# Kernel optimization log

Hardware: AMD Instinct MI355X
Metric: run time of the kernel (lower is better)

## Reference

```python
import jax, jax.numpy as jnp
import numpy as np

NEG_INF = -1e30

def setup_inputs() -> dict:
    key = jax.random.key(0)
    ks = jax.random.split(key, 8)
    B, M, d_q, d_t, d_attn = 2048, 200, 512, 768, 64
    q_vec = jax.random.normal(ks[0], (B, d_q), dtype=jnp.float32)
    desc_tokens = jax.random.normal(ks[1], (B, M, d_t), dtype=jnp.float32)
    desc_mask = jax.random.randint(ks[2], (B, M), 0, 2, dtype=jnp.int32)
    # parameters (Linear weights stored as (in, out) for x @ W)
    Wq = jax.random.normal(ks[3], (d_q, d_attn), dtype=jnp.float32) / np.sqrt(d_q)
    Wk = jax.random.normal(ks[4], (d_t, d_attn), dtype=jnp.float32) / np.sqrt(d_t)
    Wv = jax.random.normal(ks[5], (d_t, d_attn), dtype=jnp.float32) / np.sqrt(d_t)
    U = jax.random.normal(ks[6], (d_attn, d_attn), dtype=jnp.float32) / np.sqrt(d_attn)
    Wo = jax.random.normal(ks[7], (d_attn, d_q), dtype=jnp.float32) / np.sqrt(d_attn)
    bo = jnp.zeros((d_q,), dtype=jnp.float32)
    return {"q_vec": q_vec, "desc_tokens": desc_tokens, "desc_mask": desc_mask,
            "Wq": Wq, "Wk": Wk, "Wv": Wv, "U": U, "Wo": Wo, "bo": bo}

def reference(q_vec, desc_tokens, desc_mask, Wq, Wk, Wv, U, Wo, bo):
    Q = q_vec @ Wq                                   # (B, d_attn)
    K = jnp.einsum('bmt,ta->bma', desc_tokens, Wk)   # (B, M, d_attn)
    V = jnp.einsum('bmt,ta->bma', desc_tokens, Wv)   # (B, M, d_attn)
    QU = Q @ U                                       # (B, d_attn)
    scores = jnp.einsum('bd,bmd->bm', QU, K)         # (B, M)
    scores = jnp.where(desc_mask == 0, NEG_INF, scores)
    attn = jax.nn.softmax(scores, axis=-1)           # (B, M)
    context = jnp.einsum('bm,bmd->bd', attn, V)      # (B, d_attn)
    fused = context @ Wo + bo + q_vec                # (B, d_q)
    return (fused, attn)
```

## Files before the change

### kernel.cpp

```cpp
#include <hip/hip_runtime.h>
#include <math.h>

#define B_    2048
#define M_    200
#define DQ_   512
#define DT_   768
#define DA_   64
#define NEG_INF_ (-1e30f)

typedef float f4 __attribute__((ext_vector_type(4)));

__device__ __forceinline__ float dot4f(f4 a, f4 b) {
    return a[0]*b[0] + a[1]*b[1] + a[2]*b[2] + a[3]*b[3];
}
__device__ __forceinline__ void fma4(f4& a, float e, f4 c) {
    a[0] += e*c[0]; a[1] += e*c[1]; a[2] += e*c[2]; a[3] += e*c[3];
}
__device__ __forceinline__ void scale_add4(f4& a, float sc, f4 c) {
    a[0] = a[0]*sc + c[0]; a[1] = a[1]*sc + c[1];
    a[2] = a[2]*sc + c[2]; a[3] = a[3]*sc + c[3];
}

__global__ __launch_bounds__(256, 4)
void bilinear_attn_fused(const float* __restrict__ q_vec,
                         const float* __restrict__ desc,
                         const int*   __restrict__ mask,
                         const float* __restrict__ Wq,
                         const float* __restrict__ Wk,
                         const float* __restrict__ Wv,
                         const float* __restrict__ U,
                         const float* __restrict__ Wo,
                         const float* __restrict__ bo,
                         float* __restrict__ out_fused,
                         float* __restrict__ out_attn)
{
    const int b    = blockIdx.x;
    const int tid  = threadIdx.x;
    const int lane = tid & 63;
    const int wv_  = tid >> 6;

    __shared__ float s_qv[DQ_];
    __shared__ float s_red[256];
    __shared__ float s_Q[DA_];
    __shared__ float s_QU[DA_];
    __shared__ float s_w[DT_];
    __shared__ int   s_idx[M_];
    __shared__ float s_sc[M_];
    __shared__ int   s_cnt;
    __shared__ float s_wm[4], s_wl[4];
    __shared__ float s_acc[4][DT_];
    __shared__ float s_ctx[DA_];

    const float* qrow  = q_vec + (size_t)b * DQ_;
    const int*   maskb = mask  + (size_t)b * M_;

    if (wv_ == 0) {
        int total = 0;
        #pragma unroll
        for (int base = 0; base < 256; base += 64) {
            const int m  = base + lane;
            const int mk = (m < M_) ? maskb[m] : 0;
            const unsigned long long bal = __ballot(mk != 0);
            const int pre = __popcll(bal & ((1ull << lane) - 1ull));
            if (mk) s_idx[total + pre] = m;
            total += __popcll(bal);
        }
        if (lane == 0) s_cnt = total;
    } else {
        for (int i = tid - 64; i < DQ_; i += 192) s_qv[i] = qrow[i];
    }
    for (int m = tid; m < M_; m += 256) s_sc[m] = NEG_INF_;
    __syncthreads();

    {
        const int d  = lane;
        const int t0 = wv_ * (DQ_ / 4);
        float p = 0.f;
        for (int t = t0; t < t0 + DQ_ / 4; ++t)
            p += s_qv[t] * Wq[t * DA_ + d];
        s_red[tid] = p;
    }
    __syncthreads();
    if (tid < DA_)
        s_Q[tid] = s_red[tid] + s_red[tid + 64] + s_red[tid + 128] + s_red[tid + 192];
    __syncthreads();

    if (tid < DA_) {
        float qu = 0.f;
        for (int e = 0; e < DA_; ++e) qu += s_Q[e] * U[e * DA_ + tid];
        s_QU[tid] = qu;
    }
    __syncthreads();

    for (int t = tid; t < DT_; t += 256) {
        const f4* wk4 = (const f4*)(Wk + (size_t)t * DA_);
        const f4* qu4 = (const f4*)s_QU;
        float a = 0.f;
        #pragma unroll
        for (int i = 0; i < DA_ / 4; ++i) a += dot4f(wk4[i], qu4[i]);
        s_w[t] = a;
    }
    __syncthreads();

    const int off0 = lane * 4, off1 = lane * 4 + 256, off2 = lane * 4 + 512;
    const f4 w0 = *(const f4*)&s_w[off0];
    const f4 w1 = *(const f4*)&s_w[off1];
    const f4 w2 = *(const f4*)&s_w[off2];

    const float* descb = desc + (size_t)b * M_ * DT_;
    const int    Nu    = s_cnt;

    f4 acc0 = {0,0,0,0}, acc1 = {0,0,0,0}, acc2 = {0,0,0,0};
    float mw = -INFINITY, lw = 0.f;

    f4 c0 = {0,0,0,0}, c1 = {0,0,0,0}, c2 = {0,0,0,0};
    if (wv_ < Nu) {
        const float* r = descb + (size_t)s_idx[wv_] * DT_;
        c0 = *(const f4*)(r + off0);
        c1 = *(const f4*)(r + off1);
        c2 = *(const f4*)(r + off2);
    }
    for (int j = wv_; j < Nu; j += 4) {
        const int row = s_idx[j];
        f4 n0 = {0,0,0,0}, n1 = {0,0,0,0}, n2 = {0,0,0,0};
        const int nj = j + 4;
        if (nj < Nu) {
            const float* r = descb + (size_t)s_idx[nj] * DT_;
            n0 = *(const f4*)(r + off0);
            n1 = *(const f4*)(r + off1);
            n2 = *(const f4*)(r + off2);
        }
        float p = dot4f(c0, w0) + dot4f(c1, w1) + dot4f(c2, w2);
        #pragma unroll
        for (int o = 32; o >= 1; o >>= 1) p += __shfl_xor(p, o, 64);
        if (lane == 0) s_sc[row] = p;

        if (p <= mw) {
            const float e = __expf(p - mw);
            lw += e;
            fma4(acc0, e, c0); fma4(acc1, e, c1); fma4(acc2, e, c2);
        } else {
            const float sc = __expf(mw - p);
            lw = lw * sc + 1.f;
            scale_add4(acc0, sc, c0); scale_add4(acc1, sc, c1); scale_add4(acc2, sc, c2);
            mw = p;
        }
        c0 = n0; c1 = n1; c2 = n2;
    }

    if (lane == 0) { s_wm[wv_] = mw; s_wl[wv_] = lw; }
    *(f4*)&s_acc[wv_][off0] = acc0;
    *(f4*)&s_acc[wv_][off1] = acc1;
    *(f4*)&s_acc[wv_][off2] = acc2;
    __syncthreads();

    const float m0 = s_wm[0], m1 = s_wm[1], m2 = s_wm[2], m3 = s_wm[3];
    const float Mx = fmaxf(fmaxf(fmaxf(m0, m1), fmaxf(m2, m3)), -3.0e29f);
    const float f0 = __expf(m0 - Mx), f1 = __expf(m1 - Mx);
    const float f2 = __expf(m2 - Mx), f3 = __expf(m3 - Mx);
    const float ltot  = s_wl[0]*f0 + s_wl[1]*f1 + s_wl[2]*f2 + s_wl[3]*f3;
    const float inv_l = (ltot > 0.f) ? (1.0f / ltot) : 0.f;

    for (int t = tid; t < DT_; t += 256) {
        const float v = s_acc[0][t]*f0 + s_acc[1][t]*f1
                      + s_acc[2][t]*f2 + s_acc[3][t]*f3;
        s_acc[0][t] = v * inv_l;
    }
    for (int m = tid; m < M_; m += 256)
        out_attn[(size_t)b * M_ + m] = __expf(s_sc[m] - Mx) * inv_l;
    __syncthreads();

    {
        const int d  = lane;
        const int t0 = wv_ * (DT_ / 4);
        float cp = 0.f;
        for (int t = t0; t < t0 + DT_ / 4; ++t)
            cp += s_acc[0][t] * Wv[(size_t)t * DA_ + d];
        s_red[tid] = cp;
    }
    __syncthreads();
    if (tid < DA_)
        s_ctx[tid] = s_red[tid] + s_red[tid + 64] + s_red[tid + 128] + s_red[tid + 192];
    __syncthreads();

    for (int j = tid; j < DQ_; j += 256) {
        float f = bo[j] + s_qv[j];
        #pragma unroll 8
        for (int d = 0; d < DA_; ++d)
            f += s_ctx[d] * Wo[(size_t)d * DQ_ + j];
        out_fused[(size_t)b * DQ_ + j] = f;
    }
}

extern "C" void kernel_launch(void* const* d_in, const int* in_sizes, int n_in,
                              void* d_out, int out_size, void* d_ws, size_t ws_size,
                              hipStream_t stream) {
    (void)in_sizes; (void)n_in; (void)d_ws; (void)ws_size; (void)out_size;

    const float* q_vec = (const float*)d_in[0];
    const float* desc  = (const float*)d_in[1];
    const int*   mask  = (const int*)  d_in[2];
    const float* Wq    = (const float*)d_in[3];
    const float* Wk    = (const float*)d_in[4];
    const float* Wv    = (const float*)d_in[5];
    const float* U     = (const float*)d_in[6];
    const float* Wo    = (const float*)d_in[7];
    const float* bo    = (const float*)d_in[8];

    float* out_fused = (float*)d_out;
    float* out_attn  = (float*)d_out + (size_t)B_ * DQ_;

    bilinear_attn_fused<<<dim3(B_), dim3(256), 0, stream>>>(
        q_vec, desc, mask, Wq, Wk, Wv, U, Wo, bo, out_fused, out_attn);
}
```

Baseline: 196.1 us.

## Split each wavefront into half-waves processing two rows concurrently

New measurement: 194.1 us. Within noise of the previous version (-1.0%).

```diff
diff --git a/kernel.cpp b/kernel.cpp
--- a/kernel.cpp
+++ b/kernel.cpp
@@ -7,18 +7,12 @@
 #define DT_   768
 #define DA_   64
 #define NEG_INF_ (-1e30f)
+#define MINIT_  (-3.0e29f)
 
 typedef float f4 __attribute__((ext_vector_type(4)));
 
 __device__ __forceinline__ float dot4f(f4 a, f4 b) {
     return a[0]*b[0] + a[1]*b[1] + a[2]*b[2] + a[3]*b[3];
-}
-__device__ __forceinline__ void fma4(f4& a, float e, f4 c) {
-    a[0] += e*c[0]; a[1] += e*c[1]; a[2] += e*c[2]; a[3] += e*c[3];
-}
-__device__ __forceinline__ void scale_add4(f4& a, float sc, f4 c) {
-    a[0] = a[0]*sc + c[0]; a[1] = a[1]*sc + c[1];
-    a[2] = a[2]*sc + c[2]; a[3] = a[3]*sc + c[3];
 }
 
 __global__ __launch_bounds__(256, 4)
@@ -38,6 +32,8 @@
     const int tid  = threadIdx.x;
     const int lane = tid & 63;
     const int wv_  = tid >> 6;
+    const int half = lane >> 5;
+    const int hl   = lane & 31;
 
     __shared__ float s_qv[DQ_];
     __shared__ float s_red[256];
@@ -47,8 +43,8 @@
     __shared__ int   s_idx[M_];
     __shared__ float s_sc[M_];
     __shared__ int   s_cnt;
-    __shared__ float s_wm[4], s_wl[4];
-    __shared__ float s_acc[4][DT_];
+    __shared__ float s_wm[8], s_wl[8];
+    __shared__ float s_acc[8][DT_];
     __shared__ float s_ctx[DA_];
 
     const float* qrow  = q_vec + (size_t)b * DQ_;
@@ -102,68 +98,94 @@
     }
     __syncthreads();
 
-    const int off0 = lane * 4, off1 = lane * 4 + 256, off2 = lane * 4 + 512;
-    const f4 w0 = *(const f4*)&s_w[off0];
-    const f4 w1 = *(const f4*)&s_w[off1];
-    const f4 w2 = *(const f4*)&s_w[off2];
+    f4 wr[6];
+    #pragma unroll
+    for (int j = 0; j < 6; ++j)
+        wr[j] = *(const f4*)&s_w[hl * 4 + j * 128];
 
     const float* descb = desc + (size_t)b * M_ * DT_;
     const int    Nu    = s_cnt;
-
-    f4 acc0 = {0,0,0,0}, acc1 = {0,0,0,0}, acc2 = {0,0,0,0};
-    float mw = -INFINITY, lw = 0.f;
-
-    f4 c0 = {0,0,0,0}, c1 = {0,0,0,0}, c2 = {0,0,0,0};
-    if (wv_ < Nu) {
-        const float* r = descb + (size_t)s_idx[wv_] * DT_;
-        c0 = *(const f4*)(r + off0);
-        c1 = *(const f4*)(r + off1);
-        c2 = *(const f4*)(r + off2);
-    }
-    for (int j = wv_; j < Nu; j += 4) {
-        const int row = s_idx[j];
-        f4 n0 = {0,0,0,0}, n1 = {0,0,0,0}, n2 = {0,0,0,0};
-        const int nj = j + 4;
-        if (nj < Nu) {
-            const float* r = descb + (size_t)s_idx[nj] * DT_;
-            n0 = *(const f4*)(r + off0);
-            n1 = *(const f4*)(r + off1);
-            n2 = *(const f4*)(r + off2);
+    const int    npairs = (Nu + 1) >> 1;
+
+    f4 acc[6] = {{0,0,0,0},{0,0,0,0},{0,0,0,0},{0,0,0,0},{0,0,0,0},{0,0,0,0}};
+    float mw = MINIT_, lw = 0.f;
+
+    if (Nu > 0) {
+        const int last = Nu - 1;
+        int rid;
+        f4  c[6];
+        {
+            const int rp = 2 * wv_ + half;
+            rid = s_idx[rp < last ? rp : last];
+            const float* r = descb + (size_t)rid * DT_ + hl * 4;
+            #pragma unroll
+            for (int j = 0; j < 6; ++j) c[j] = *(const f4*)(r + j * 128);
         }
-        float p = dot4f(c0, w0) + dot4f(c1, w1) + dot4f(c2, w2);
+        for (int pp = wv_; pp < npairs; pp += 4) {
+            const bool havenext = (pp + 4) < npairs;
+            int nrid = 0;
+            f4  n[6];
+            if (havenext) {
+                const int nrp = 2 * (pp + 4) + half;
+                nrid = s_idx[nrp < last ? nrp : last];
+                const float* r = descb + (size_t)nrid * DT_ + hl * 4;
+                #pragma unroll
+                for (int j = 0; j < 6; ++j) n[j] = *(const f4*)(r + j * 128);
+            }
+
+            float p = dot4f(c[0], wr[0]) + dot4f(c[1], wr[1]) + dot4f(c[2], wr[2])
+                    + dot4f(c[3], wr[3]) + dot4f(c[4], wr[4]) + dot4f(c[5], wr[5]);
+            #pragma unroll
+            for (int o = 16; o >= 1; o >>= 1) p += __shfl_xor(p, o, 64);
+
+            const int  rpcur = 2 * pp + half;
+            const bool valid = rpcur < Nu;
+            if (hl == 0 && valid) s_sc[rid] = p;
+            const float s = valid ? p : NEG_INF_;
+
+            const float newm = fmaxf(mw, s);
+            const float e  = __expf(s - newm);
+            const float sc = __expf(mw - newm);
+            lw = lw * sc + e;
+            #pragma unroll
+            for (int j = 0; j < 6; ++j) {
+                acc[j][0] = acc[j][0] * sc + e * c[j][0];
+                acc[j][1] = acc[j][1] * sc + e * c[j][1];
+                acc[j][2] = acc[j][2] * sc + e * c[j][2];
+                acc[j][3] = acc[j][3] * sc + e * c[j][3];
+            }
+            mw = newm;
+
+            if (havenext) {
+                #pragma unroll
+                for (int j = 0; j < 6; ++j) c[j] = n[j];
+                rid = nrid;
+            }
+        }
+    }
+
+    const int hs = (wv_ << 1) | half;
+    if (hl == 0) { s_wm[hs] = mw; s_wl[hs] = lw; }
+    #pragma unroll
+    for (int j = 0; j < 6; ++j)
+        *(f4*)&s_acc[hs][hl * 4 + j * 128] = acc[j];
+    __syncthreads();
+
+    float Mx = MINIT_;
+    #pragma unroll
+    for (int i = 0; i < 8; ++i) Mx = fmaxf(Mx, s_wm[i]);
+    float fm[8], ltot = 0.f;
+    #pragma unroll
+    for (int i = 0; i < 8; ++i) {
+        fm[i] = __expf(s_wm[i] - Mx);
+        ltot += s_wl[i] * fm[i];
+    }
+    const float inv_l = (ltot > 0.f) ? (1.0f / ltot) : 0.f;
+
+    for (int t = tid; t < DT_; t += 256) {
+        float v = 0.f;
         #pragma unroll
-        for (int o = 32; o >= 1; o >>= 1) p += __shfl_xor(p, o, 64);
-        if (lane == 0) s_sc[row] = p;
-
-        if (p <= mw) {
-            const float e = __expf(p - mw);
-            lw += e;
-            fma4(acc0, e, c0); fma4(acc1, e, c1); fma4(acc2, e, c2);
-        } else {
-            const float sc = __expf(mw - p);
-            lw = lw * sc + 1.f;
-            scale_add4(acc0, sc, c0); scale_add4(acc1, sc, c1); scale_add4(acc2, sc, c2);
-            mw = p;
-        }
-        c0 = n0; c1 = n1; c2 = n2;
-    }
-
-    if (lane == 0) { s_wm[wv_] = mw; s_wl[wv_] = lw; }
-    *(f4*)&s_acc[wv_][off0] = acc0;
-    *(f4*)&s_acc[wv_][off1] = acc1;
-    *(f4*)&s_acc[wv_][off2] = acc2;
-    __syncthreads();
-
-    const float m0 = s_wm[0], m1 = s_wm[1], m2 = s_wm[2], m3 = s_wm[3];
-    const float Mx = fmaxf(fmaxf(fmaxf(m0, m1), fmaxf(m2, m3)), -3.0e29f);
-    const float f0 = __expf(m0 - Mx), f1 = __expf(m1 - Mx);
-    const float f2 = __expf(m2 - Mx), f3 = __expf(m3 - Mx);
-    const float ltot  = s_wl[0]*f0 + s_wl[1]*f1 + s_wl[2]*f2 + s_wl[3]*f3;
-    const float inv_l = (ltot > 0.f) ? (1.0f / ltot) : 0.f;
-
-    for (int t = tid; t < DT_; t += 256) {
-        const float v = s_acc[0][t]*f0 + s_acc[1][t]*f1
-                      + s_acc[2][t]*f2 + s_acc[3][t]*f3;
+        for (int i = 0; i < 8; ++i) v += s_acc[i][t] * fm[i];
         s_acc[0][t] = v * inv_l;
     }
     for (int m = tid; m < M_; m += 256)
```

## Split prologue into batched prep kernel and slimmer streaming attention kernel

Applied to the files above, without the earlier changes.

Measured after the change: 190.4 us. 1.03x faster.

```diff
diff --git a/kernel.cpp b/kernel.cpp
--- a/kernel.cpp
+++ b/kernel.cpp
@@ -6,55 +6,69 @@
 #define DQ_   512
 #define DT_   768
 #define DA_   64
+#define G_    4
 #define NEG_INF_ (-1e30f)
+#define MINIT_  (-3.0e29f)
 
 typedef float f4 __attribute__((ext_vector_type(4)));
 
 __device__ __forceinline__ float dot4f(f4 a, f4 b) {
     return a[0]*b[0] + a[1]*b[1] + a[2]*b[2] + a[3]*b[3];
 }
-__device__ __forceinline__ void fma4(f4& a, float e, f4 c) {
-    a[0] += e*c[0]; a[1] += e*c[1]; a[2] += e*c[2]; a[3] += e*c[3];
-}
-__device__ __forceinline__ void scale_add4(f4& a, float sc, f4 c) {
-    a[0] = a[0]*sc + c[0]; a[1] = a[1]*sc + c[1];
-    a[2] = a[2]*sc + c[2]; a[3] = a[3]*sc + c[3];
-}
-
-__global__ __launch_bounds__(256, 4)
-void bilinear_attn_fused(const float* __restrict__ q_vec,
-                         const float* __restrict__ desc,
-                         const int*   __restrict__ mask,
-                         const float* __restrict__ Wq,
-                         const float* __restrict__ Wk,
-                         const float* __restrict__ Wv,
-                         const float* __restrict__ U,
-                         const float* __restrict__ Wo,
-                         const float* __restrict__ bo,
-                         float* __restrict__ out_fused,
-                         float* __restrict__ out_attn)
+
+__global__ __launch_bounds__(256)
+void prep_kernel(const float* __restrict__ q_vec, const int* __restrict__ mask,
+                 const float* __restrict__ Wq, const float* __restrict__ U,
+                 const float* __restrict__ Wk,
+                 float* __restrict__ w_ws, int* __restrict__ idx_ws,
+                 int* __restrict__ cnt_ws)
 {
-    const int b    = blockIdx.x;
     const int tid  = threadIdx.x;
     const int lane = tid & 63;
-    const int wv_  = tid >> 6;
-
-    __shared__ float s_qv[DQ_];
-    __shared__ float s_red[256];
-    __shared__ float s_Q[DA_];
-    __shared__ float s_QU[DA_];
-    __shared__ float s_w[DT_];
-    __shared__ int   s_idx[M_];
-    __shared__ float s_sc[M_];
-    __shared__ int   s_cnt;
-    __shared__ float s_wm[4], s_wl[4];
-    __shared__ float s_acc[4][DT_];
-    __shared__ float s_ctx[DA_];
-
-    const float* qrow  = q_vec + (size_t)b * DQ_;
-    const int*   maskb = mask  + (size_t)b * M_;
-
-    if (wv_ == 0) {
+    const int wv   = tid >> 6;
+    const int b0   = blockIdx.x * G_;
+
+    __shared__ float s_qv[G_][DQ_];
+    __shared__ float s_Q[G_][DA_];
+    __shared__ float s_QU[G_][DA_];
+
+    for (int i = tid; i < G_ * DQ_; i += 256)
+        ((float*)s_qv)[i] = q_vec[(size_t)b0 * DQ_ + i];
+    __syncthreads();
+
+    {
+        const int g = tid >> 6, d = tid & 63;
+        float p = 0.f;
+        for (int t = 0; t < DQ_; ++t) p += s_qv[g][t] * Wq[t * DA_ + d];
+        s_Q[g][d] = p;
+    }
+    __syncthreads();
+    {
+        const int g = tid >> 6, d = tid & 63;
+        float qu = 0.f;
+        for (int e = 0; e < DA_; ++e) qu += s_Q[g][e] * U[e * DA_ + d];
+        s_QU[g][d] = qu;
+    }
+    __syncthreads();
+    for (int t = tid; t < DT_; t += 256) {
+        const f4* wk4 = (const f4*)(Wk + (size_t)t * DA_);
+        float a0 = 0.f, a1 = 0.f, a2 = 0.f, a3 = 0.f;
+        #pragma unroll
+        for (int i = 0; i < DA_ / 4; ++i) {
+            const f4 kk = wk4[i];
+            a0 += dot4f(kk, *(const f4*)&s_QU[0][i * 4]);
+            a1 += dot4f(kk, *(const f4*)&s_QU[1][i * 4]);
+            a2 += dot4f(kk, *(const f4*)&s_QU[2][i * 4]);
+            a3 += dot4f(kk, *(const f4*)&s_QU[3][i * 4]);
+        }
+        w_ws[(size_t)(b0 + 0) * DT_ + t] = a0;
+        w_ws[(size_t)(b0 + 1) * DT_ + t] = a1;
+        w_ws[(size_t)(b0 + 2) * DT_ + t] = a2;
+        w_ws[(size_t)(b0 + 3) * DT_ + t] = a3;
+    }
+    {
+        const int b = b0 + wv;
+        const int* maskb = mask + (size_t)b * M_;
         int total = 0;
         #pragma unroll
         for (int base = 0; base < 256; base += 64) {
@@ -62,120 +76,99 @@
             const int mk = (m < M_) ? maskb[m] : 0;
             const unsigned long long bal = __ballot(mk != 0);
             const int pre = __popcll(bal & ((1ull << lane) - 1ull));
-            if (mk) s_idx[total + pre] = m;
+            if (mk) idx_ws[(size_t)b * M_ + total + pre] = m;
             total += __popcll(bal);
         }
-        if (lane == 0) s_cnt = total;
-    } else {
-        for (int i = tid - 64; i < DQ_; i += 192) s_qv[i] = qrow[i];
-    }
+        if (lane == 0) cnt_ws[b] = total;
+    }
+}
+
+__global__ __launch_bounds__(256, 8)
+void stream_kernel(const float* __restrict__ desc,
+                   const float* __restrict__ w_ws,
+                   const int*   __restrict__ idx_ws,
+                   const int*   __restrict__ cnt_ws,
+                   const float* __restrict__ q_vec,
+                   const float* __restrict__ Wv,
+                   const float* __restrict__ Wo,
+                   const float* __restrict__ bo,
+                   float* __restrict__ out_fused,
+                   float* __restrict__ out_attn)
+{
+    const int b    = blockIdx.x;
+    const int tid  = threadIdx.x;
+    const int lane = tid & 63;
+    const int wv   = tid >> 6;
+
+    __shared__ int   s_idx[M_];
+    __shared__ float s_sc[M_];
+    __shared__ float s_acc[4][DT_];
+    __shared__ float s_red[256];
+    __shared__ float s_wm[4], s_wl[4];
+    __shared__ float s_ctx[DA_];
+
+    const int Nu = cnt_ws[b];
     for (int m = tid; m < M_; m += 256) s_sc[m] = NEG_INF_;
-    __syncthreads();
-
-    {
-        const int d  = lane;
-        const int t0 = wv_ * (DQ_ / 4);
-        float p = 0.f;
-        for (int t = t0; t < t0 + DQ_ / 4; ++t)
-            p += s_qv[t] * Wq[t * DA_ + d];
-        s_red[tid] = p;
-    }
-    __syncthreads();
-    if (tid < DA_)
-        s_Q[tid] = s_red[tid] + s_red[tid + 64] + s_red[tid + 128] + s_red[tid + 192];
-    __syncthreads();
-
-    if (tid < DA_) {
-        float qu = 0.f;
-        for (int e = 0; e < DA_; ++e) qu += s_Q[e] * U[e * DA_ + tid];
-        s_QU[tid] = qu;
-    }
-    __syncthreads();
-
-    for (int t = tid; t < DT_; t += 256) {
-        const f4* wk4 = (const f4*)(Wk + (size_t)t * DA_);
-        const f4* qu4 = (const f4*)s_QU;
-        float a = 0.f;
-        #pragma unroll
-        for (int i = 0; i < DA_ / 4; ++i) a += dot4f(wk4[i], qu4[i]);
-        s_w[t] = a;
-    }
-    __syncthreads();
-
-    const int off0 = lane * 4, off1 = lane * 4 + 256, off2 = lane * 4 + 512;
-    const f4 w0 = *(const f4*)&s_w[off0];
-    const f4 w1 = *(const f4*)&s_w[off1];
-    const f4 w2 = *(const f4*)&s_w[off2];
-
-    const float* descb = desc + (size_t)b * M_ * DT_;
-    const int    Nu    = s_cnt;
-
-    f4 acc0 = {0,0,0,0}, acc1 = {0,0,0,0}, acc2 = {0,0,0,0};
-    float mw = -INFINITY, lw = 0.f;
-
-    f4 c0 = {0,0,0,0}, c1 = {0,0,0,0}, c2 = {0,0,0,0};
-    if (wv_ < Nu) {
-        const float* r = descb + (size_t)s_idx[wv_] * DT_;
-        c0 = *(const f4*)(r + off0);
-        c1 = *(const f4*)(r + off1);
-        c2 = *(const f4*)(r + off2);
-    }
-    for (int j = wv_; j < Nu; j += 4) {
-        const int row = s_idx[j];
-        f4 n0 = {0,0,0,0}, n1 = {0,0,0,0}, n2 = {0,0,0,0};
-        const int nj = j + 4;
-        if (nj < Nu) {
-            const float* r = descb + (size_t)s_idx[nj] * DT_;
-            n0 = *(const f4*)(r + off0);
-            n1 = *(const f4*)(r + off1);
-            n2 = *(const f4*)(r + off2);
-        }
+    for (int m = tid; m < Nu; m += 256) s_idx[m] = idx_ws[(size_t)b * M_ + m];
+
+    const float* wrow = w_ws + (size_t)b * DT_ + lane * 4;
+    const f4 w0 = *(const f4*)(wrow);
+    const f4 w1 = *(const f4*)(wrow + 256);
+    const f4 w2 = *(const f4*)(wrow + 512);
+    __syncthreads();
+
+    f4 a0 = {0,0,0,0}, a1 = {0,0,0,0}, a2 = {0,0,0,0};
+    float mw = MINIT_, lw = 0.f;
+
+    const float* descb = desc + (size_t)b * (M_ * DT_) + lane * 4;
+
+    for (int j = wv; j < Nu; j += 4) {
+        const int rid = s_idx[j];
+        const float* r = descb + (size_t)rid * DT_;
+        const f4 c0 = *(const f4*)(r);
+        const f4 c1 = *(const f4*)(r + 256);
+        const f4 c2 = *(const f4*)(r + 512);
+
         float p = dot4f(c0, w0) + dot4f(c1, w1) + dot4f(c2, w2);
         #pragma unroll
         for (int o = 32; o >= 1; o >>= 1) p += __shfl_xor(p, o, 64);
-        if (lane == 0) s_sc[row] = p;
-
-        if (p <= mw) {
-            const float e = __expf(p - mw);
-            lw += e;
-            fma4(acc0, e, c0); fma4(acc1, e, c1); fma4(acc2, e, c2);
-        } else {
-            const float sc = __expf(mw - p);
-            lw = lw * sc + 1.f;
-            scale_add4(acc0, sc, c0); scale_add4(acc1, sc, c1); scale_add4(acc2, sc, c2);
-            mw = p;
-        }
-        c0 = n0; c1 = n1; c2 = n2;
-    }
-
-    if (lane == 0) { s_wm[wv_] = mw; s_wl[wv_] = lw; }
-    *(f4*)&s_acc[wv_][off0] = acc0;
-    *(f4*)&s_acc[wv_][off1] = acc1;
-    *(f4*)&s_acc[wv_][off2] = acc2;
+        if (lane == 0) s_sc[rid] = p;
+
+        const float newm = fmaxf(mw, p);
+        const float e  = __expf(p - newm);
+        const float sc = __expf(mw - newm);
+        lw = lw * sc + e;
+        a0 = a0 * sc + e * c0;
+        a1 = a1 * sc + e * c1;
+        a2 = a2 * sc + e * c2;
+        mw = newm;
+    }
+
+    if (lane == 0) { s_wm[wv] = mw; s_wl[wv] = lw; }
+    *(f4*)&s_acc[wv][lane * 4]       = a0;
+    *(f4*)&s_acc[wv][lane * 4 + 256] = a1;
+    *(f4*)&s_acc[wv][lane * 4 + 512] = a2;
     __syncthreads();
 
     const float m0 = s_wm[0], m1 = s_wm[1], m2 = s_wm[2], m3 = s_wm[3];
-    const float Mx = fmaxf(fmaxf(fmaxf(m0, m1), fmaxf(m2, m3)), -3.0e29f);
+    const float Mx = fmaxf(fmaxf(m0, m1), fmaxf(m2, m3));
     const float f0 = __expf(m0 - Mx), f1 = __expf(m1 - Mx);
     const float f2 = __expf(m2 - Mx), f3 = __expf(m3 - Mx);
     const float ltot  = s_wl[0]*f0 + s_wl[1]*f1 + s_wl[2]*f2 + s_wl[3]*f3;
     const float inv_l = (ltot > 0.f) ? (1.0f / ltot) : 0.f;
 
-    for (int t = tid; t < DT_; t += 256) {
-        const float v = s_acc[0][t]*f0 + s_acc[1][t]*f1
-                      + s_acc[2][t]*f2 + s_acc[3][t]*f3;
-        s_acc[0][t] = v * inv_l;
-    }
+    for (int t = tid; t < DT_; t += 256)
+        s_acc[0][t] = (s_acc[0][t]*f0 + s_acc[1][t]*f1
+                     + s_acc[2][t]*f2 + s_acc[3][t]*f3) * inv_l;
     for (int m = tid; m < M_; m += 256)
         out_attn[(size_t)b * M_ + m] = __expf(s_sc[m] - Mx) * inv_l;
     __syncthreads();
 
     {
-        const int d  = lane;
-        const int t0 = wv_ * (DT_ / 4);
+        const int t0 = wv * (DT_ / 4);
         float cp = 0.f;
         for (int t = t0; t < t0 + DT_ / 4; ++t)
-            cp += s_acc[0][t] * Wv[(size_t)t * DA_ + d];
+            cp += s_acc[0][t] * Wv[(size_t)t * DA_ + lane];
         s_red[tid] = cp;
     }
     __syncthreads();
@@ -183,19 +176,20 @@
         s_ctx[tid] = s_red[tid] + s_red[tid + 64] + s_red[tid + 128] + s_red[tid + 192];
     __syncthreads();
 
-    for (int j = tid; j < DQ_; j += 256) {
-        float f = bo[j] + s_qv[j];
+    const float* qrow = q_vec + (size_t)b * DQ_;
+    for (int jq = tid; jq < DQ_; jq += 256) {
+        float f = bo[jq] + qrow[jq];
         #pragma unroll 8
         for (int d = 0; d < DA_; ++d)
-            f += s_ctx[d] * Wo[(size_t)d * DQ_ + j];
-        out_fused[(size_t)b * DQ_ + j] = f;
+            f += s_ctx[d] * Wo[(size_t)d * DQ_ + jq];
+        out_fused[(size_t)b * DQ_ + jq] = f;
     }
 }
 
 extern "C" void kernel_launch(void* const* d_in, const int* in_sizes, int n_in,
                               void* d_out, int out_size, void* d_ws, size_t ws_size,
                               hipStream_t stream) {
-    (void)in_sizes; (void)n_in; (void)d_ws; (void)ws_size; (void)out_size;
+    (void)in_sizes; (void)n_in; (void)ws_size; (void)out_size;
 
     const float* q_vec = (const float*)d_in[0];
     const float* desc  = (const float*)d_in[1];
@@ -210,6 +204,13 @@
     float* out_fused = (float*)d_out;
     float* out_attn  = (float*)d_out + (size_t)B_ * DQ_;
 
-    bilinear_attn_fused<<<dim3(B_), dim3(256), 0, stream>>>(
-        q_vec, desc, mask, Wq, Wk, Wv, U, Wo, bo, out_fused, out_attn);
-}
+    float* w_ws   = (float*)d_ws;
+    int*   idx_ws = (int*)((char*)d_ws + (size_t)B_ * DT_ * sizeof(float));
+    int*   cnt_ws = idx_ws + (size_t)B_ * M_;
+
+    prep_kernel<<<dim3(B_ / G_), dim3(256), 0, stream>>>(
+        q_vec, mask, Wq, U, Wk, w_ws, idx_ws, cnt_ws);
+
+    stream_kernel<<<dim3(B_), dim3(256), 0, stream>>>(
+        desc, w_ws, idx_ws, cnt_ws, q_vec, Wv, Wo, bo, out_fused, out_attn);
+}
```
